# Kernel optimization log

Hardware: AMD Instinct MI355X
Metric: run time of the kernel (lower is better)

The kernel has to match this reference:

```python
import jax, jax.numpy as jnp
import numpy as np

B, L, D = 32, 256, 512
D_STATE, D_CONV, EXPAND, NODE_DIM, D_FF = 16, 4, 2, 16, 2048
D_INNER = EXPAND * D
DT_RANK = D // 16


def _layernorm(x, g, b, eps=1e-5):
    mu = x.mean(-1, keepdims=True)
    var = ((x - mu) ** 2).mean(-1, keepdims=True)
    return (x - mu) * jax.lax.rsqrt(var + eps) * g + b


def _mamba(x, in_w, conv_w, conv_b, xproj_w, dt_w, dt_b, A_log, Dp, out_w):
    # Standard selective-scan (S6) Mamba inner block.
    Bb, Ll, _ = x.shape
    u, z = jnp.split(x @ in_w, 2, axis=-1)                # (B,L,d_inner) each
    pad = jnp.pad(u, ((0, 0), (D_CONV - 1, 0), (0, 0)))   # causal depthwise conv1d
    u = sum(pad[:, k:k + Ll, :] * conv_w[:, k] for k in range(D_CONV)) + conv_b
    u = jax.nn.silu(u)
    proj = u @ xproj_w                                    # (B,L,dt_rank+2*d_state)
    dt, Bm, Cm = jnp.split(proj, [DT_RANK, DT_RANK + D_STATE], axis=-1)
    dt = jax.nn.softplus(dt @ dt_w + dt_b)                # (B,L,d_inner)
    A = -jnp.exp(A_log)                                   # (d_inner,d_state)
    dA = jnp.exp(dt[..., None] * A)                       # (B,L,d_inner,d_state)
    dBu = dt[..., None] * Bm[:, :, None, :] * u[..., None]

    def step(h, inp):
        dA_t, dBu_t, C_t = inp
        h = dA_t * h + dBu_t
        return h, jnp.einsum('bds,bs->bd', h, C_t)

    h0 = jnp.zeros((Bb, D_INNER, D_STATE), x.dtype)
    _, ys = jax.lax.scan(step, h0, (dA.transpose(1, 0, 2, 3),
                                    dBu.transpose(1, 0, 2, 3),
                                    Cm.transpose(1, 0, 2)))
    y = ys.transpose(1, 0, 2) + u * Dp                    # (B,L,d_inner)
    return (y * jax.nn.silu(z)) @ out_w


def _forward(x,
             d_in_w, d_conv_w, d_conv_b, d_xproj_w, d_dt_w, d_dt_b, d_A_log, d_D, d_out_w, d_ln_g, d_ln_b,
             s_emb1, s_emb2, s_in_w, s_conv_w, s_conv_b, s_xproj_w, s_dt_w, s_dt_b, s_A_log, s_D, s_out_w, s_ln_g, s_ln_b,
             f_ln_g, f_ln_b, f_w1, f_b1, f_w2, f_b2):
    # DiffSSM: selective SSM on the first-differenced sequence, residual + LN
    xd = jnp.concatenate([x[:, :1], x[:, 1:] - x[:, :-1]], axis=1)
    x = _layernorm(x + _mamba(xd, d_in_w, d_conv_w, d_conv_b, d_xproj_w,
                              d_dt_w, d_dt_b, d_A_log, d_D, d_out_w),
                   d_ln_g, d_ln_b)
    # SpatialGraphMamba: learned adjacency over enc_in tokens, graph mix, SSM
    adj = jax.nn.softmax(jax.nn.relu(s_emb1 @ s_emb2.T), axis=-1)  # (enc_in,enc_in)
    xg = jnp.einsum('nl,bld->bnd', adj, x)
    x = _layernorm(x + _mamba(xg, s_in_w, s_conv_w, s_conv_b, s_xproj_w,
                              s_dt_w, s_dt_b, s_A_log, s_D, s_out_w),
                   s_ln_g, s_ln_b)
    # Pre-norm FFN with residual
    h = _layernorm(x, f_ln_g, f_ln_b)
    x = x + jax.nn.gelu(h @ f_w1 + f_b1) @ f_w2 + f_b2
    return x, adj


def setup_inputs() -> dict:
    key = jax.random.key(0)
    ks = iter(jax.random.split(key, 64))

    def rn(shape, s=0.02):
        return jax.random.normal(next(ks), shape, jnp.float32) * s

    A_log_init = jnp.log(jnp.broadcast_to(
        jnp.arange(1, D_STATE + 1, dtype=jnp.float32), (D_INNER, D_STATE)))
    dt_b_init = jnp.full((D_INNER,), -4.6, jnp.float32)  # softplus^-1(~0.01)

    inp = {'x': jax.random.normal(next(ks), (B, L, D), jnp.float32)}
    for p in ('d_', 's_'):
        inp[p + 'in_w'] = rn((D, 2 * D_INNER))
        inp[p + 'conv_w'] = rn((D_INNER, D_CONV), 0.1)
        inp[p + 'conv_b'] = jnp.zeros((D_INNER,), jnp.float32)
        inp[p + 'xproj_w'] = rn((D_INNER, DT_RANK + 2 * D_STATE))
        inp[p + 'dt_w'] = rn((DT_RANK, D_INNER))
        inp[p + 'dt_b'] = dt_b_init
        inp[p + 'A_log'] = A_log_init
        inp[p + 'D'] = jnp.ones((D_INNER,), jnp.float32)
        inp[p + 'out_w'] = rn((D_INNER, D))
        inp[p + 'ln_g'] = jnp.ones((D,), jnp.float32)
        inp[p + 'ln_b'] = jnp.zeros((D,), jnp.float32)
    inp['s_emb1'] = rn((L, NODE_DIM), 0.1)
    inp['s_emb2'] = rn((L, NODE_DIM), 0.1)
    inp['f_ln_g'] = jnp.ones((D,), jnp.float32)
    inp['f_ln_b'] = jnp.zeros((D,), jnp.float32)
    inp['f_w1'] = rn((D, D_FF))
    inp['f_b1'] = jnp.zeros((D_FF,), jnp.float32)
    inp['f_w2'] = rn((D_FF, D))
    inp['f_b2'] = jnp.zeros((D,), jnp.float32)
    return inp


def reference(x,
              d_in_w, d_conv_w, d_conv_b, d_xproj_w, d_dt_w, d_dt_b, d_A_log, d_D, d_out_w, d_ln_g, d_ln_b,
              s_emb1, s_emb2, s_in_w, s_conv_w, s_conv_b, s_xproj_w, s_dt_w, s_dt_b, s_A_log, s_D, s_out_w, s_ln_g, s_ln_b,
              f_ln_g, f_ln_b, f_w1, f_b1, f_w2, f_b2):
    return _forward(x,
                    d_in_w, d_conv_w, d_conv_b, d_xproj_w, d_dt_w, d_dt_b, d_A_log, d_D, d_out_w, d_ln_g, d_ln_b,
                    s_emb1, s_emb2, s_in_w, s_conv_w, s_conv_b, s_xproj_w, s_dt_w, s_dt_b, s_A_log, s_D, s_out_w, s_ln_g, s_ln_b,
                    f_ln_g, f_ln_b, f_w1, f_b1, f_w2, f_b2)
```

## Files before the change

### kernel.cpp

```cpp
#include <hip/hip_runtime.h>

#define DEV __device__ __forceinline__

typedef __bf16 bf16x8 __attribute__((ext_vector_type(8)));
typedef float  f32x4  __attribute__((ext_vector_type(4)));

DEV unsigned short f2b(float f) {
    union { float f; unsigned u; } v; v.f = f;
    unsigned r = v.u + 0x7fffu + ((v.u >> 16) & 1u);
    return (unsigned short)(r >> 16);
}
DEV float b2f(unsigned short h) {
    union { unsigned u; float f; } v; v.u = ((unsigned)h) << 16;
    return v.f;
}
DEV float sigmoidf_(float x) { return 1.f / (1.f + __expf(-x)); }
DEV float geluf_(float x) {
    float t = 0.7978845608028654f * (x + 0.044715f * x * x * x);
    return 0.5f * x * (1.f + tanhf(t));
}
DEV float softplusf_(float x) { return x > 15.f ? x : log1pf(__expf(x)); }
DEV void gload_lds16(const void* g, void* l) {
    __builtin_amdgcn_global_load_lds((const __attribute__((address_space(1))) void*)g,
                                     (__attribute__((address_space(3))) void*)l, 16, 0, 0);
}


struct WtDesc { const float* s; unsigned short* d; int K; int N; int t0; };
struct WtArgs { WtDesc m[12]; };

__global__ __launch_bounds__(256) void wtrans_k(WtArgs a) {
    __shared__ float tile[32][33];
    int t = blockIdx.x;
    int mi = 0;
#pragma unroll
    for (int j = 1; j < 12; j++) if (t >= a.m[j].t0) mi = j;
    const float* src0 = a.m[mi].s;
    unsigned short* dst0 = a.m[mi].d;
    const int K = a.m[mi].K, N = a.m[mi].N;
    const int lt = t - a.m[mi].t0;
    const int ntk = K >> 5;
    const int kt = lt % ntk, nt = lt / ntk;
    const int c = threadIdx.x & 31, r = threadIdx.x >> 5;
    const float* src = src0 + (size_t)(kt * 32) * N + nt * 32;
#pragma unroll
    for (int i = 0; i < 4; i++) tile[r + i * 8][c] = src[(size_t)(r + i * 8) * N + c];
    __syncthreads();
    unsigned short* dst = dst0 + (size_t)(nt * 32) * K + kt * 32;
#pragma unroll
    for (int i = 0; i < 4; i++) dst[(size_t)(r + i * 8) * K + c] = f2b(tile[c][r + i * 8]);
}

__global__ __launch_bounds__(256) void diff_k(const float* __restrict__ x,
                                              unsigned short* __restrict__ xd) {
    size_t i4 = (size_t)blockIdx.x * 256 + threadIdx.x;
    size_t idx = i4 * 4;
    int l = (int)((idx >> 9) & 255);
    float4 v = *(const float4*)&x[idx];
    if (l > 0) {
        float4 p = *(const float4*)&x[idx - 512];
        v.x -= p.x; v.y -= p.y; v.z -= p.z; v.w -= p.w;
    }
    unsigned short o[4] = {f2b(v.x), f2b(v.y), f2b(v.z), f2b(v.w)};
    *(unsigned long long*)&xd[idx] = *(unsigned long long*)o;
}

__global__ __launch_bounds__(256) void adj_k(const float* __restrict__ e1,
                                             const float* __restrict__ e2,
                                             float* __restrict__ adjf,
                                             unsigned short* __restrict__ adjb) {
    const int n = blockIdx.x, tid = threadIdx.x;
    __shared__ float e1s[16];
    __shared__ float redm[4], reds[4];
    if (tid < 16) e1s[tid] = e1[n * 16 + tid];
    __syncthreads();
    const float* e2r = e2 + tid * 16;
    float dot = 0.f;
#pragma unroll
    for (int k = 0; k < 16; k++) dot = fmaf(e1s[k], e2r[k], dot);
    float v = fmaxf(dot, 0.f);
    float m = v;
#pragma unroll
    for (int o = 32; o > 0; o >>= 1) m = fmaxf(m, __shfl_xor(m, o));
    const int lane = tid & 63, wv = tid >> 6;
    if (lane == 0) redm[wv] = m;
    __syncthreads();
    m = fmaxf(fmaxf(redm[0], redm[1]), fmaxf(redm[2], redm[3]));
    float e = __expf(v - m);
    float ssum = e;
#pragma unroll
    for (int o = 32; o > 0; o >>= 1) ssum += __shfl_xor(ssum, o);
    if (lane == 0) reds[wv] = ssum;
    __syncthreads();
    ssum = reds[0] + reds[1] + reds[2] + reds[3];
    float o = e / ssum;
    adjf[(size_t)n * 256 + tid] = o;
    adjb[(size_t)n * 256 + tid] = f2b(o);
}

template<int BM, int BN, int BK, int WRN, int FM, int FN,
         int OBF, int HBIAS, int HGELU, int HRES, int HSP>
__global__ __launch_bounds__(256) void gemm_k(
    const unsigned short* __restrict__ A, const unsigned short* __restrict__ Bt,
    void* __restrict__ C, const float* __restrict__ bias, const float* __restrict__ res,
    int M, int N, int K, int lda, long sA, long sB, long sC) {
    constexpr int SMASK = BK / 8 - 1;
    constexpr int KH    = BK / 32;
    constexpr int AI = (BM * BK) / 2048;
    constexpr int BI = (BN * BK) / 2048;
    __shared__ __align__(16) unsigned short As[2][BM * BK];
    __shared__ __align__(16) unsigned short Bs[2][BN * BK];
    const int tid  = threadIdx.x;
    const int lane = tid & 63;
    const int wave = tid >> 6;
    const int wr = wave / WRN, wc = wave % WRN;
    const int bm = blockIdx.x * BM, bn = blockIdx.y * BN;
    const unsigned short* Ab = A  + (size_t)blockIdx.z * sA;
    const unsigned short* Bb = Bt + (size_t)blockIdx.z * sB;
    const int lrow  = lane & 15;
    const int klane = lane >> 4;

    f32x4 acc[FM][FN];
#pragma unroll
    for (int m = 0; m < FM; m++)
#pragma unroll
        for (int n = 0; n < FN; n++) {
            acc[m][n][0] = 0.f; acc[m][n][1] = 0.f; acc[m][n][2] = 0.f; acc[m][n][3] = 0.f;
        }

    auto STAGE = [&](int buf, int k0) {
#pragma unroll
        for (int it = 0; it < AI; ++it) {
            int flat = (it * 256 + tid) * 8;
            int r = flat / BK, s = (flat % BK) >> 3;
            int c = (s ^ (r & SMASK)) * 8;
            gload_lds16(Ab + (size_t)(bm + r) * lda + (k0 + c),
                        &As[buf][(it * 256 + (tid & 192)) * 8]);
        }
#pragma unroll
        for (int it = 0; it < BI; ++it) {
            int flat = (it * 256 + tid) * 8;
            int r = flat / BK, s = (flat % BK) >> 3;
            int c = (s ^ (r & SMASK)) * 8;
            gload_lds16(Bb + (size_t)(bn + r) * K + (k0 + c),
                        &Bs[buf][(it * 256 + (tid & 192)) * 8]);
        }
    };
    auto COMPUTE = [&](int buf) {
#pragma unroll
        for (int kk = 0; kk < KH; kk++) {
            bf16x8 af[FM], bfv[FN];
#pragma unroll
            for (int m = 0; m < FM; m++) {
                int rr = wr * FM * 16 + m * 16 + lrow;
                int sl = (kk * 4 + klane) ^ (rr & SMASK);
                af[m] = *(const bf16x8*)&As[buf][rr * BK + sl * 8];
            }
#pragma unroll
            for (int n = 0; n < FN; n++) {
                int rr = wc * FN * 16 + n * 16 + lrow;
                int sl = (kk * 4 + klane) ^ (rr & SMASK);
                bfv[n] = *(const bf16x8*)&Bs[buf][rr * BK + sl * 8];
            }
#pragma unroll
            for (int m = 0; m < FM; m++)
#pragma unroll
                for (int n = 0; n < FN; n++)
                    acc[m][n] = __builtin_amdgcn_mfma_f32_16x16x32_bf16(af[m], bfv[n], acc[m][n], 0, 0, 0);
        }
    };

    const int nt = K / BK;
    STAGE(0, 0);
    __syncthreads();
    for (int t = 0; t < nt; t += 2) {
        if (t + 1 < nt) STAGE(1, (t + 1) * BK);
        COMPUTE(0);
        __syncthreads();
        if (t + 1 < nt) {
            if (t + 2 < nt) STAGE(0, (t + 2) * BK);
            COMPUTE(1);
            if (t + 2 < nt) __syncthreads();
        }
    }

    const int r0 = (lane >> 4) << 2;
    if (OBF) {
        unsigned short* Cs = Bs[0];
        constexpr int PITCH = BN + 8;
        unsigned short* Cg = (unsigned short*)C;
#pragma unroll
        for (int g = 0; g < BM / 32; g++) {
            __syncthreads();
            if (wr == (g * 2) / FM) {
                const int mb = (g * 2) % FM;
#pragma unroll
                for (int mm = 0; mm < 2; mm++) {
#pragma unroll
                    for (int n = 0; n < FN; n++) {
                        const int cl = wc * FN * 16 + n * 16 + lrow;
                        float bv = HBIAS ? bias[bn + cl] : 0.f;
#pragma unroll
                        for (int j = 0; j < 4; j++) {
                            float v = acc[mb + mm][n][j] + bv;
                            if (HSP)   v = softplusf_(v);
                            if (HGELU) v = geluf_(v);
                            Cs[(mm * 16 + r0 + j) * PITCH + cl] = f2b(v);
                        }
                    }
                }
            }
            __syncthreads();
#pragma unroll
            for (int i = 0; i < (32 * BN) / 2048; i++) {
                int flat = (i * 256 + tid) * 8;
                int row = flat / BN, col = flat % BN;
                uint4 val = *(const uint4*)&Cs[row * PITCH + col];
                size_t oi = (size_t)blockIdx.z * sC + (size_t)(bm + g * 32 + row) * N + bn + col;
                *(uint4*)&Cg[oi] = val;
            }
        }
    } else {
#pragma unroll
        for (int n = 0; n < FN; n++) {
            const int ccol = bn + wc * FN * 16 + n * 16 + lrow;
            float bv = HBIAS ? bias[ccol] : 0.f;
#pragma unroll
            for (int m = 0; m < FM; m++) {
#pragma unroll
                for (int j = 0; j < 4; j++) {
                    const int rrow = bm + wr * FM * 16 + m * 16 + r0 + j;
                    float v = acc[m][n][j] + bv;
                    if (HSP)   v = softplusf_(v);
                    if (HGELU) v = geluf_(v);
                    if (HRES)  v += res[(size_t)rrow * N + ccol];
                    ((float*)C)[(size_t)blockIdx.z * sC + (size_t)rrow * N + ccol] = v;
                }
            }
        }
    }
}

__global__ __launch_bounds__(256) void conv_k(const unsigned short* __restrict__ uz,
                                              const float* __restrict__ w,
                                              const float* __restrict__ cb,
                                              unsigned short* __restrict__ u) {
    int t = blockIdx.x * 256 + threadIdx.x;
    int dg = t & 127;
    size_t row = (size_t)(t >> 7);
    int l = (int)(row & 255);
    int d0 = dg * 8;
    float acc[8];
#pragma unroll
    for (int j = 0; j < 8; j++) acc[j] = cb[d0 + j];
#pragma unroll
    for (int k = 0; k < 4; k++) {
        int ls = l + k - 3;
        if (ls >= 0) {
            const unsigned short* src = uz + (((size_t)row + k - 3) << 11) + d0;
            uint4 v = *(const uint4*)src;
            const unsigned short* vs = (const unsigned short*)&v;
#pragma unroll
            for (int j = 0; j < 8; j++)
                acc[j] = fmaf(w[(d0 + j) * 4 + k], b2f(vs[j]), acc[j]);
        }
    }
    unsigned short o[8];
#pragma unroll
    for (int j = 0; j < 8; j++) {
        float a = acc[j];
        o[j] = f2b(a * sigmoidf_(a));
    }
    *(uint4*)(u + (row << 10) + d0) = *(const uint4*)o;
}

__global__ __launch_bounds__(256) void scan1_k(
    const float* __restrict__ dt,
    const unsigned short* __restrict__ u,
    const unsigned short* __restrict__ proj,
    const float* __restrict__ A_log,
    float* __restrict__ hend, float* __restrict__ Sc) {
    const int dg = blockIdx.x, c = blockIdx.y, b = blockIdx.z;
    const int d = dg * 256 + threadIdx.x;
    const size_t base = (size_t)b * 256 + c * 32;
    __shared__ float Bs[32][16];
    for (int i = threadIdx.x; i < 512; i += 256) {
        int r = i >> 4, s = i & 15;
        Bs[r][s] = b2f(proj[(base + r) * 64 + 32 + s]);
    }
    __syncthreads();
    float Aa[16];
#pragma unroll
    for (int s = 0; s < 16; s++) Aa[s] = -__expf(A_log[d * 16 + s]);
    float h[16];
#pragma unroll
    for (int s = 0; s < 16; s++) h[s] = 0.f;
    float ssum = 0.f;
    for (int l = 0; l < 32; l++) {
        size_t row = base + l;
        float dtv = dt[(row << 10) + d];
        float uu  = b2f(u[(row << 10) + d]);
        float du  = dtv * uu;
        ssum += dtv;
#pragma unroll
        for (int s = 0; s < 16; s++)
            h[s] = __expf(dtv * Aa[s]) * h[s] + du * Bs[l][s];
    }
    size_t o = (size_t)(b * 8 + c) * 1024 + d;
    Sc[o] = ssum;
#pragma unroll
    for (int s = 0; s < 16; s++) hend[o * 16 + s] = h[s];
}

__global__ __launch_bounds__(256) void scan2_k(
    const float* __restrict__ hend, const float* __restrict__ Sc,
    const float* __restrict__ A_log, float* __restrict__ hstart) {
    const int d = blockIdx.x * 256 + threadIdx.x;
    const int b = blockIdx.y;
    float Aa[16];
#pragma unroll
    for (int s = 0; s < 16; s++) Aa[s] = -__expf(A_log[d * 16 + s]);
    float h[16];
#pragma unroll
    for (int s = 0; s < 16; s++) h[s] = 0.f;
    for (int c = 0; c < 8; c++) {
        size_t o = (size_t)(b * 8 + c) * 1024 + d;
#pragma unroll
        for (int s = 0; s < 16; s++) hstart[o * 16 + s] = h[s];
        float sc = Sc[o];
#pragma unroll
        for (int s = 0; s < 16; s++)
            h[s] = __expf(sc * Aa[s]) * h[s] + hend[o * 16 + s];
    }
}

__global__ __launch_bounds__(256) void scan3_k(
    const float* __restrict__ dt,
    const unsigned short* __restrict__ u,
    const unsigned short* __restrict__ uz,
    const unsigned short* __restrict__ proj,
    const float* __restrict__ A_log,
    const float* __restrict__ Dp,
    const float* __restrict__ hstart,
    unsigned short* __restrict__ yg) {
    const int dg = blockIdx.x, c = blockIdx.y, b = blockIdx.z;
    const int d = dg * 256 + threadIdx.x;
    const size_t base = (size_t)b * 256 + c * 32;
    __shared__ float BCs[32][32];
    for (int i = threadIdx.x; i < 1024; i += 256) {
        int r = i >> 5, s = i & 31;
        BCs[r][s] = b2f(proj[(base + r) * 64 + 32 + s]);
    }
    __syncthreads();
    float Aa[16];
#pragma unroll
    for (int s = 0; s < 16; s++) Aa[s] = -__expf(A_log[d * 16 + s]);
    const float Dd = Dp[d];
    float h[16];
    size_t ho = ((size_t)(b * 8 + c) * 1024 + d) * 16;
#pragma unroll
    for (int s = 0; s < 16; s++) h[s] = hstart[ho + s];
    for (int l = 0; l < 32; l++) {
        size_t row = base + l;
        float dtv = dt[(row << 10) + d];
        float uu  = b2f(u[(row << 10) + d]);
        float zz  = b2f(uz[(row << 11) + 1024 + d]);
        float du  = dtv * uu;
        float y = 0.f;
#pragma unroll
        for (int s = 0; s < 16; s++) {
            h[s] = __expf(dtv * Aa[s]) * h[s] + du * BCs[l][s];
            y = fmaf(h[s], BCs[l][16 + s], y);
        }
        y = fmaf(uu, Dd, y);
        yg[(row << 10) + d] = f2b(y * (zz * sigmoidf_(zz)));
    }
}

template<int HRES, int OF32, int OBF>
__global__ __launch_bounds__(256) void ln_k(const float* __restrict__ xin,
                                            const float* __restrict__ resin,
                                            const float* __restrict__ g,
                                            const float* __restrict__ b,
                                            float* __restrict__ outf,
                                            unsigned short* __restrict__ outb) {
    const int row = blockIdx.x, tid = threadIdx.x;
    float2 v = ((const float2*)(xin + (size_t)row * 512))[tid];
    if (HRES) {
        float2 r2 = ((const float2*)(resin + (size_t)row * 512))[tid];
        v.x += r2.x; v.y += r2.y;
    }
    float s = v.x + v.y, q = v.x * v.x + v.y * v.y;
#pragma unroll
    for (int o = 32; o > 0; o >>= 1) { s += __shfl_xor(s, o); q += __shfl_xor(q, o); }
    __shared__ float sm[4], qm[4];
    const int lane = tid & 63, wv = tid >> 6;
    if (lane == 0) { sm[wv] = s; qm[wv] = q; }
    __syncthreads();
    s = sm[0] + sm[1] + sm[2] + sm[3];
    q = qm[0] + qm[1] + qm[2] + qm[3];
    const float mu = s * (1.f / 512.f);
    const float ri = rsqrtf(q * (1.f / 512.f) - mu * mu + 1e-5f);
    float2 gg = ((const float2*)g)[tid];
    float2 bb = ((const float2*)b)[tid];
    float o0 = (v.x - mu) * ri * gg.x + bb.x;
    float o1 = (v.y - mu) * ri * gg.y + bb.y;
    if (OF32) ((float2*)(outf + (size_t)row * 512))[tid] = make_float2(o0, o1);
    if (OBF) {
        unsigned short* ob = outb + (size_t)row * 512 + tid * 2;
        ob[0] = f2b(o0); ob[1] = f2b(o1);
    }
}

__global__ __launch_bounds__(256) void trans_k(const float* __restrict__ x1,
                                               unsigned short* __restrict__ xt) {
    __shared__ float tile[32][33];
    const int b = blockIdx.z;
    const int d0 = blockIdx.x * 32, l0 = blockIdx.y * 32;
    const int c = threadIdx.x & 31, r = threadIdx.x >> 5;
    const float* src = x1 + ((size_t)b * 256 + l0) * 512 + d0;
#pragma unroll
    for (int i = 0; i < 4; i++) tile[r + i * 8][c] = src[(size_t)(r + i * 8) * 512 + c];
    __syncthreads();
    unsigned short* dst = xt + ((size_t)b * 512 + d0) * 256 + l0;
#pragma unroll
    for (int i = 0; i < 4; i++) dst[(size_t)(r + i * 8) * 256 + c] = f2b(tile[c][r + i * 8]);
}

constexpr size_t OFF_WT_DIN  = 0;
constexpr size_t OFF_WT_SIN  = OFF_WT_DIN  + 2048ull * 512 * 2;
constexpr size_t OFF_WT_DOUT = OFF_WT_SIN  + 2048ull * 512 * 2;
constexpr size_t OFF_WT_SOUT = OFF_WT_DOUT + 512ull * 1024 * 2;
constexpr size_t OFF_WT_F1   = OFF_WT_SOUT + 512ull * 1024 * 2;
constexpr size_t OFF_WT_F2   = OFF_WT_F1   + 2048ull * 512 * 2;
constexpr size_t OFF_XPT_D   = OFF_WT_F2   + 512ull * 2048 * 2;
constexpr size_t OFF_XPT_S   = OFF_XPT_D   + 64ull * 1024 * 2;
constexpr size_t OFF_DTT_D   = OFF_XPT_S   + 64ull * 1024 * 2;
constexpr size_t OFF_DTT_S   = OFF_DTT_D   + 1024ull * 32 * 2;
constexpr size_t OFF_ACT     = OFF_DTT_S   + 1024ull * 32 * 2;
constexpr size_t OFF_UZ      = OFF_ACT  + 8192ull * 512 * 2;
constexpr size_t OFF_U       = OFF_UZ   + 8192ull * 2048 * 2;
constexpr size_t OFF_PROJ    = OFF_U    + 8192ull * 1024 * 2;
constexpr size_t OFF_YG      = OFF_PROJ + 8192ull * 64 * 2;
constexpr size_t OFF_MOUT    = OFF_YG   + 8192ull * 1024 * 2;
constexpr size_t OFF_X1      = OFF_MOUT + 8192ull * 512 * 4;
constexpr size_t OFF_X2      = OFF_X1   + 8192ull * 512 * 4;
constexpr size_t OFF_X1T     = OFF_X2   + 8192ull * 512 * 4;
constexpr size_t OFF_ADJB    = OFF_X1T  + 32ull * 512 * 256 * 2;
constexpr size_t OFF_DT      = OFF_ADJB + 256ull * 256 * 2;
constexpr size_t OFF_HST     = OFF_DT   + 8192ull * 1024 * 4;
constexpr size_t OFF_SC      = OFF_HST  + 32ull * 8 * 1024 * 16 * 4;

extern "C" void kernel_launch(void* const* d_in, const int* in_sizes, int n_in,
                              void* d_out, int out_size, void* d_ws, size_t ws_size,
                              hipStream_t stream) {
    (void)in_sizes; (void)n_in; (void)out_size; (void)ws_size;
    const float* x      = (const float*)d_in[0];
    const float* dinw   = (const float*)d_in[1];
    const float* dconvw = (const float*)d_in[2];
    const float* dconvb = (const float*)d_in[3];
    const float* dxproj = (const float*)d_in[4];
    const float* ddtw   = (const float*)d_in[5];
    const float* ddtb   = (const float*)d_in[6];
    const float* dAlog  = (const float*)d_in[7];
    const float* dD     = (const float*)d_in[8];
    const float* doutw  = (const float*)d_in[9];
    const float* dlng   = (const float*)d_in[10];
    const float* dlnb   = (const float*)d_in[11];
    const float* sinw   = (const float*)d_in[12];
    const float* sconvw = (const float*)d_in[13];
    const float* sconvb = (const float*)d_in[14];
    const float* sxproj = (const float*)d_in[15];
    const float* sdtw   = (const float*)d_in[16];
    const float* sdtb   = (const float*)d_in[17];
    const float* sAlog  = (const float*)d_in[18];
    const float* sD     = (const float*)d_in[19];
    const float* soutw  = (const float*)d_in[20];
    const float* slng   = (const float*)d_in[21];
    const float* slnb   = (const float*)d_in[22];
    const float* semb1  = (const float*)d_in[23];
    const float* semb2  = (const float*)d_in[24];
    const float* flng   = (const float*)d_in[25];
    const float* flnb   = (const float*)d_in[26];
    const float* fw1    = (const float*)d_in[27];
    const float* fb1    = (const float*)d_in[28];
    const float* fw2    = (const float*)d_in[29];
    const float* fb2    = (const float*)d_in[30];

    char* ws = (char*)d_ws;
    unsigned short* wtDin  = (unsigned short*)(ws + OFF_WT_DIN);
    unsigned short* wtSin  = (unsigned short*)(ws + OFF_WT_SIN);
    unsigned short* wtDout = (unsigned short*)(ws + OFF_WT_DOUT);
    unsigned short* wtSout = (unsigned short*)(ws + OFF_WT_SOUT);
    unsigned short* wtF1   = (unsigned short*)(ws + OFF_WT_F1);
    unsigned short* wtF2   = (unsigned short*)(ws + OFF_WT_F2);
    unsigned short* xptD   = (unsigned short*)(ws + OFF_XPT_D);
    unsigned short* xptS   = (unsigned short*)(ws + OFF_XPT_S);
    unsigned short* dttD   = (unsigned short*)(ws + OFF_DTT_D);
    unsigned short* dttS   = (unsigned short*)(ws + OFF_DTT_S);
    unsigned short* actIn  = (unsigned short*)(ws + OFF_ACT);
    unsigned short* uzBuf  = (unsigned short*)(ws + OFF_UZ);
    unsigned short* uBuf   = (unsigned short*)(ws + OFF_U);
    unsigned short* projB  = (unsigned short*)(ws + OFF_PROJ);
    unsigned short* ygBuf  = (unsigned short*)(ws + OFF_YG);
    float*          moutB  = (float*)(ws + OFF_MOUT);
    float*          hendB  = moutB;
    float*          x1Buf  = (float*)(ws + OFF_X1);
    float*          x2Buf  = (float*)(ws + OFF_X2);
    unsigned short* x1tBuf = (unsigned short*)(ws + OFF_X1T);
    unsigned short* adjB   = (unsigned short*)(ws + OFF_ADJB);
    float*          dtBuf  = (float*)(ws + OFF_DT);
    float*          hstB   = (float*)(ws + OFF_HST);
    float*          scB    = (float*)(ws + OFF_SC);
    unsigned short* hBuf   = uBuf;
    unsigned short* midBuf = uzBuf;

    float* outX   = (float*)d_out;
    float* outAdj = outX + 4194304;

    WtArgs wa;
    wa.m[0]  = WtDesc{dinw,   wtDin,  512,  2048, 0};
    wa.m[1]  = WtDesc{sinw,   wtSin,  512,  2048, 1024};
    wa.m[2]  = WtDesc{doutw,  wtDout, 1024, 512,  2048};
    wa.m[3]  = WtDesc{soutw,  wtSout, 1024, 512,  2560};
    wa.m[4]  = WtDesc{fw1,    wtF1,   512,  2048, 3072};
    wa.m[5]  = WtDesc{fw2,    wtF2,   2048, 512,  4096};
    wa.m[6]  = WtDesc{dxproj, xptD,   1024, 64,   5120};
    wa.m[7]  = WtDesc{sxproj, xptS,   1024, 64,   5184};
    wa.m[8]  = WtDesc{ddtw,   dttD,   32,   1024, 5248};
    wa.m[9]  = WtDesc{sdtw,   dttS,   32,   1024, 5280};
    wa.m[10] = WtDesc{dinw,   wtDin,  512,  2048, 0x7fffffff};
    wa.m[11] = WtDesc{dinw,   wtDin,  512,  2048, 0x7fffffff};
    wtrans_k<<<dim3(5312), dim3(256), 0, stream>>>(wa);

    diff_k<<<dim3(4096), dim3(256), 0, stream>>>(x, actIn);
    adj_k<<<dim3(256), dim3(256), 0, stream>>>(semb1, semb2, outAdj, adjB);

    gemm_k<128,128,64,2,4,4, 1,0,0,0,0><<<dim3(64,16,1), dim3(256), 0, stream>>>(
        actIn, wtDin, uzBuf, nullptr, nullptr, 8192, 2048, 512, 512, 0, 0, 0);
    conv_k<<<dim3(4096), dim3(256), 0, stream>>>(uzBuf, dconvw, dconvb, uBuf);
    gemm_k<64,64,64,2,2,2, 1,0,0,0,0><<<dim3(128,1,1), dim3(256), 0, stream>>>(
        uBuf, xptD, projB, nullptr, nullptr, 8192, 64, 1024, 1024, 0, 0, 0);
    gemm_k<128,128,32,2,4,4, 0,1,0,0,1><<<dim3(64,8,1), dim3(256), 0, stream>>>(
        projB, dttD, dtBuf, ddtb, nullptr, 8192, 1024, 32, 64, 0, 0, 0);
    scan1_k<<<dim3(4,8,32), dim3(256), 0, stream>>>(dtBuf, uBuf, projB, dAlog, hendB, scB);
    scan2_k<<<dim3(4,32),   dim3(256), 0, stream>>>(hendB, scB, dAlog, hstB);
    scan3_k<<<dim3(4,8,32), dim3(256), 0, stream>>>(dtBuf, uBuf, uzBuf, projB, dAlog, dD, hstB, ygBuf);
    gemm_k<128,128,64,2,4,4, 0,0,0,0,0><<<dim3(64,4,1), dim3(256), 0, stream>>>(
        ygBuf, wtDout, moutB, nullptr, nullptr, 8192, 512, 1024, 1024, 0, 0, 0);
    ln_k<1,1,0><<<dim3(8192), dim3(256), 0, stream>>>(moutB, x, dlng, dlnb, x1Buf, nullptr);

    trans_k<<<dim3(16,8,32), dim3(256), 0, stream>>>(x1Buf, x1tBuf);
    gemm_k<128,128,64,2,4,4, 1,0,0,0,0><<<dim3(2,4,32), dim3(256), 0, stream>>>(
        adjB, x1tBuf, actIn, nullptr, nullptr, 256, 512, 256, 256, 0, 131072, 131072);
    gemm_k<128,128,64,2,4,4, 1,0,0,0,0><<<dim3(64,16,1), dim3(256), 0, stream>>>(
        actIn, wtSin, uzBuf, nullptr, nullptr, 8192, 2048, 512, 512, 0, 0, 0);
    conv_k<<<dim3(4096), dim3(256), 0, stream>>>(uzBuf, sconvw, sconvb, uBuf);
    gemm_k<64,64,64,2,2,2, 1,0,0,0,0><<<dim3(128,1,1), dim3(256), 0, stream>>>(
        uBuf, xptS, projB, nullptr, nullptr, 8192, 64, 1024, 1024, 0, 0, 0);
    gemm_k<128,128,32,2,4,4, 0,1,0,0,1><<<dim3(64,8,1), dim3(256), 0, stream>>>(
        projB, dttS, dtBuf, sdtb, nullptr, 8192, 1024, 32, 64, 0, 0, 0);
    scan1_k<<<dim3(4,8,32), dim3(256), 0, stream>>>(dtBuf, uBuf, projB, sAlog, hendB, scB);
    scan2_k<<<dim3(4,32),   dim3(256), 0, stream>>>(hendB, scB, sAlog, hstB);
    scan3_k<<<dim3(4,8,32), dim3(256), 0, stream>>>(dtBuf, uBuf, uzBuf, projB, sAlog, sD, hstB, ygBuf);
    gemm_k<128,128,64,2,4,4, 0,0,0,0,0><<<dim3(64,4,1), dim3(256), 0, stream>>>(
        ygBuf, wtSout, moutB, nullptr, nullptr, 8192, 512, 1024, 1024, 0, 0, 0);
    ln_k<1,1,0><<<dim3(8192), dim3(256), 0, stream>>>(moutB, x1Buf, slng, slnb, x2Buf, nullptr);

    ln_k<0,0,1><<<dim3(8192), dim3(256), 0, stream>>>(x2Buf, nullptr, flng, flnb, nullptr, hBuf);
    gemm_k<128,128,64,2,4,4, 1,1,1,0,0><<<dim3(64,16,1), dim3(256), 0, stream>>>(
        hBuf, wtF1, midBuf, fb1, nullptr, 8192, 2048, 512, 512, 0, 0, 0);
    gemm_k<128,128,64,2,4,4, 0,1,0,1,0><<<dim3(64,4,1), dim3(256), 0, stream>>>(
        midBuf, wtF2, outX, fb2, x2Buf, 8192, 512, 2048, 2048, 0, 0, 0);
}
```

Measured before the change: 653.2 us.

## Add 256x256 tile GEMM for wide projections and single-buffer generic GEMM

Introduces a 512-thread 256x256x64 double-buffered GEMM kernel used for the two Mamba input projections and the first FFN layer, raising per-block data reuse. The generic GEMM kernel is changed from double-buffered LDS staging to a single buffer with a barrier after each load and compute. That cuts its LDS footprint, which may allow more resident blocks, but it loses load/compute overlap. The large kernel's 128KB LDS limits it to one block per CU.

```diff
diff --git a/kernel.cpp b/kernel.cpp
--- a/kernel.cpp
+++ b/kernel.cpp
@@ -98,6 +98,121 @@
     adjb[(size_t)n * 256 + tid] = f2b(o);
 }
 
+template<int HBIAS, int HGELU>
+__global__ __launch_bounds__(512, 2) void gemm256_k(
+    const unsigned short* __restrict__ A, const unsigned short* __restrict__ Bt,
+    unsigned short* __restrict__ C, const float* __restrict__ bias,
+    int M, int N, int K, int lda) {
+    constexpr int BM = 256, BN = 256, BK = 64;
+    __shared__ __align__(16) unsigned short As[2][BM * BK];
+    __shared__ __align__(16) unsigned short Bs[2][BN * BK];
+    const int tid  = threadIdx.x;
+    const int lane = tid & 63;
+    const int wave = tid >> 6;
+    const int wr = wave >> 2;
+    const int wc = wave & 3;
+    const int bm = blockIdx.x * BM, bn = blockIdx.y * BN;
+    const int lrow  = lane & 15;
+    const int klane = lane >> 4;
+
+    f32x4 acc[8][4];
+#pragma unroll
+    for (int m = 0; m < 8; m++)
+#pragma unroll
+        for (int n = 0; n < 4; n++) {
+            acc[m][n][0] = 0.f; acc[m][n][1] = 0.f; acc[m][n][2] = 0.f; acc[m][n][3] = 0.f;
+        }
+
+    auto STAGE = [&](int buf, int k0) {
+#pragma unroll
+        for (int it = 0; it < 4; ++it) {
+            int flat = (it * 512 + tid) * 8;
+            int r = flat >> 6, s = (flat & 63) >> 3;
+            int c = (s ^ (r & 7)) * 8;
+            gload_lds16(A + (size_t)(bm + r) * lda + (k0 + c),
+                        &As[buf][(it * 512 + (tid & 448)) * 8]);
+        }
+#pragma unroll
+        for (int it = 0; it < 4; ++it) {
+            int flat = (it * 512 + tid) * 8;
+            int r = flat >> 6, s = (flat & 63) >> 3;
+            int c = (s ^ (r & 7)) * 8;
+            gload_lds16(Bt + (size_t)(bn + r) * K + (k0 + c),
+                        &Bs[buf][(it * 512 + (tid & 448)) * 8]);
+        }
+    };
+    auto COMPUTE = [&](int buf) {
+#pragma unroll
+        for (int kk = 0; kk < 2; kk++) {
+            bf16x8 af[8], bfv[4];
+#pragma unroll
+            for (int m = 0; m < 8; m++) {
+                int rr = wr * 128 + m * 16 + lrow;
+                int sl = (kk * 4 + klane) ^ (rr & 7);
+                af[m] = *(const bf16x8*)&As[buf][rr * BK + sl * 8];
+            }
+#pragma unroll
+            for (int n = 0; n < 4; n++) {
+                int rr = wc * 64 + n * 16 + lrow;
+                int sl = (kk * 4 + klane) ^ (rr & 7);
+                bfv[n] = *(const bf16x8*)&Bs[buf][rr * BK + sl * 8];
+            }
+#pragma unroll
+            for (int m = 0; m < 8; m++)
+#pragma unroll
+                for (int n = 0; n < 4; n++)
+                    acc[m][n] = __builtin_amdgcn_mfma_f32_16x16x32_bf16(af[m], bfv[n], acc[m][n], 0, 0, 0);
+        }
+    };
+
+    const int nt = K / BK;
+    STAGE(0, 0);
+    __syncthreads();
+    for (int t = 0; t < nt; t += 2) {
+        if (t + 1 < nt) STAGE(1, (t + 1) * BK);
+        COMPUTE(0);
+        __syncthreads();
+        if (t + 1 < nt) {
+            if (t + 2 < nt) STAGE(0, (t + 2) * BK);
+            COMPUTE(1);
+            if (t + 2 < nt) __syncthreads();
+        }
+    }
+
+    const int r0 = (lane >> 4) << 2;
+    unsigned short* Cs = As[0];
+    constexpr int PITCH = BN + 8;
+#pragma unroll
+    for (int g = 0; g < 8; g++) {
+        __syncthreads();
+        if (wr == (g >> 2)) {
+#pragma unroll
+            for (int mm = 0; mm < 2; mm++) {
+                const int m = (g & 3) * 2 + mm;
+#pragma unroll
+                for (int n = 0; n < 4; n++) {
+                    const int cl = wc * 64 + n * 16 + lrow;
+                    float bv = HBIAS ? bias[bn + cl] : 0.f;
+#pragma unroll
+                    for (int j = 0; j < 4; j++) {
+                        float v = acc[m][n][j] + bv;
+                        if (HGELU) v = geluf_(v);
+                        Cs[(mm * 16 + r0 + j) * PITCH + cl] = f2b(v);
+                    }
+                }
+            }
+        }
+        __syncthreads();
+#pragma unroll
+        for (int i = 0; i < 2; i++) {
+            int flat = (i * 512 + tid) * 8;
+            int row = flat >> 8, col = flat & 255;
+            uint4 val = *(const uint4*)&Cs[row * PITCH + col];
+            *(uint4*)&C[(size_t)(bm + g * 32 + row) * N + bn + col] = val;
+        }
+    }
+}
+
 template<int BM, int BN, int BK, int WRN, int FM, int FN,
          int OBF, int HBIAS, int HGELU, int HRES, int HSP>
 __global__ __launch_bounds__(256) void gemm_k(
@@ -106,10 +221,8 @@
     int M, int N, int K, int lda, long sA, long sB, long sC) {
     constexpr int SMASK = BK / 8 - 1;
     constexpr int KH    = BK / 32;
-    constexpr int AI = (BM * BK) / 2048;
-    constexpr int BI = (BN * BK) / 2048;
-    __shared__ __align__(16) unsigned short As[2][BM * BK];
-    __shared__ __align__(16) unsigned short Bs[2][BN * BK];
+    __shared__ __align__(16) unsigned short As[BM * BK];
+    __shared__ __align__(16) unsigned short Bs[BN * BK];
     const int tid  = threadIdx.x;
     const int lane = tid & 63;
     const int wave = tid >> 6;
@@ -128,14 +241,17 @@
             acc[m][n][0] = 0.f; acc[m][n][1] = 0.f; acc[m][n][2] = 0.f; acc[m][n][3] = 0.f;
         }
 
-    auto STAGE = [&](int buf, int k0) {
+    constexpr int AI = (BM * BK) / 2048;
+    constexpr int BI = (BN * BK) / 2048;
+
+    for (int k0 = 0; k0 < K; k0 += BK) {
 #pragma unroll
         for (int it = 0; it < AI; ++it) {
             int flat = (it * 256 + tid) * 8;
             int r = flat / BK, s = (flat % BK) >> 3;
             int c = (s ^ (r & SMASK)) * 8;
             gload_lds16(Ab + (size_t)(bm + r) * lda + (k0 + c),
-                        &As[buf][(it * 256 + (tid & 192)) * 8]);
+                        &As[(it * 256 + (tid & 192)) * 8]);
         }
 #pragma unroll
         for (int it = 0; it < BI; ++it) {
@@ -143,10 +259,9 @@
             int r = flat / BK, s = (flat % BK) >> 3;
             int c = (s ^ (r & SMASK)) * 8;
             gload_lds16(Bb + (size_t)(bn + r) * K + (k0 + c),
-                        &Bs[buf][(it * 256 + (tid & 192)) * 8]);
-        }
-    };
-    auto COMPUTE = [&](int buf) {
+                        &Bs[(it * 256 + (tid & 192)) * 8]);
+        }
+        __syncthreads();
 #pragma unroll
         for (int kk = 0; kk < KH; kk++) {
             bf16x8 af[FM], bfv[FN];
@@ -154,13 +269,13 @@
             for (int m = 0; m < FM; m++) {
                 int rr = wr * FM * 16 + m * 16 + lrow;
                 int sl = (kk * 4 + klane) ^ (rr & SMASK);
-                af[m] = *(const bf16x8*)&As[buf][rr * BK + sl * 8];
+                af[m] = *(const bf16x8*)&As[rr * BK + sl * 8];
             }
 #pragma unroll
             for (int n = 0; n < FN; n++) {
                 int rr = wc * FN * 16 + n * 16 + lrow;
                 int sl = (kk * 4 + klane) ^ (rr & SMASK);
-                bfv[n] = *(const bf16x8*)&Bs[buf][rr * BK + sl * 8];
+                bfv[n] = *(const bf16x8*)&Bs[rr * BK + sl * 8];
             }
 #pragma unroll
             for (int m = 0; m < FM; m++)
@@ -168,25 +283,12 @@
                 for (int n = 0; n < FN; n++)
                     acc[m][n] = __builtin_amdgcn_mfma_f32_16x16x32_bf16(af[m], bfv[n], acc[m][n], 0, 0, 0);
         }
-    };
-
-    const int nt = K / BK;
-    STAGE(0, 0);
-    __syncthreads();
-    for (int t = 0; t < nt; t += 2) {
-        if (t + 1 < nt) STAGE(1, (t + 1) * BK);
-        COMPUTE(0);
         __syncthreads();
-        if (t + 1 < nt) {
-            if (t + 2 < nt) STAGE(0, (t + 2) * BK);
-            COMPUTE(1);
-            if (t + 2 < nt) __syncthreads();
-        }
     }
 
     const int r0 = (lane >> 4) << 2;
     if (OBF) {
-        unsigned short* Cs = Bs[0];
+        unsigned short* Cs = Bs;
         constexpr int PITCH = BN + 8;
         unsigned short* Cg = (unsigned short*)C;
 #pragma unroll
@@ -536,8 +638,8 @@
     diff_k<<<dim3(4096), dim3(256), 0, stream>>>(x, actIn);
     adj_k<<<dim3(256), dim3(256), 0, stream>>>(semb1, semb2, outAdj, adjB);
 
-    gemm_k<128,128,64,2,4,4, 1,0,0,0,0><<<dim3(64,16,1), dim3(256), 0, stream>>>(
-        actIn, wtDin, uzBuf, nullptr, nullptr, 8192, 2048, 512, 512, 0, 0, 0);
+    gemm256_k<0,0><<<dim3(32,8), dim3(512), 0, stream>>>(
+        actIn, wtDin, uzBuf, nullptr, 8192, 2048, 512, 512);
     conv_k<<<dim3(4096), dim3(256), 0, stream>>>(uzBuf, dconvw, dconvb, uBuf);
     gemm_k<64,64,64,2,2,2, 1,0,0,0,0><<<dim3(128,1,1), dim3(256), 0, stream>>>(
         uBuf, xptD, projB, nullptr, nullptr, 8192, 64, 1024, 1024, 0, 0, 0);
@@ -553,8 +655,8 @@
     trans_k<<<dim3(16,8,32), dim3(256), 0, stream>>>(x1Buf, x1tBuf);
     gemm_k<128,128,64,2,4,4, 1,0,0,0,0><<<dim3(2,4,32), dim3(256), 0, stream>>>(
         adjB, x1tBuf, actIn, nullptr, nullptr, 256, 512, 256, 256, 0, 131072, 131072);
-    gemm_k<128,128,64,2,4,4, 1,0,0,0,0><<<dim3(64,16,1), dim3(256), 0, stream>>>(
-        actIn, wtSin, uzBuf, nullptr, nullptr, 8192, 2048, 512, 512, 0, 0, 0);
+    gemm256_k<0,0><<<dim3(32,8), dim3(512), 0, stream>>>(
+        actIn, wtSin, uzBuf, nullptr, 8192, 2048, 512, 512);
     conv_k<<<dim3(4096), dim3(256), 0, stream>>>(uzBuf, sconvw, sconvb, uBuf);
     gemm_k<64,64,64,2,2,2, 1,0,0,0,0><<<dim3(128,1,1), dim3(256), 0, stream>>>(
         uBuf, xptS, projB, nullptr, nullptr, 8192, 64, 1024, 1024, 0, 0, 0);
@@ -568,8 +670,8 @@
     ln_k<1,1,0><<<dim3(8192), dim3(256), 0, stream>>>(moutB, x1Buf, slng, slnb, x2Buf, nullptr);
 
     ln_k<0,0,1><<<dim3(8192), dim3(256), 0, stream>>>(x2Buf, nullptr, flng, flnb, nullptr, hBuf);
-    gemm_k<128,128,64,2,4,4, 1,1,1,0,0><<<dim3(64,16,1), dim3(256), 0, stream>>>(
-        hBuf, wtF1, midBuf, fb1, nullptr, 8192, 2048, 512, 512, 0, 0, 0);
+    gemm256_k<1,1><<<dim3(32,8), dim3(512), 0, stream>>>(
+        hBuf, wtF1, midBuf, fb1, 8192, 2048, 512, 512);
     gemm_k<128,128,64,2,4,4, 0,1,0,1,0><<<dim3(64,4,1), dim3(256), 0, stream>>>(
         midBuf, wtF2, outX, fb2, x2Buf, 8192, 512, 2048, 2048, 0, 0, 0);
 }
```

Result: faster. 637.7 us (-2.4%).
